# Kernel tuning notes

Measured on AMD Instinct MI355X. Metric: run time of the kernel, lower is better.

The kernel has to match this reference:

```python
import jax, jax.numpy as jnp
import numpy as np

LAM = 0.1       # self.lam
MAX_ITER = 100  # fista_reweighted maxIter
TOL = 1e-5      # convergence tolerance


def creat_dictionary(T, rr, theta):
    # torch creatRealDictionary: row i = [1, rr^i*cos(i*theta), rr^i*sin(i*theta)]
    i = jnp.arange(T, dtype=rr.dtype)[:, None]           # [T,1]
    p = rr[None, :] ** i                                  # [T,P]
    W1 = p * jnp.cos(i * theta[None, :])                  # [T,P]
    W2 = p * jnp.sin(i * theta[None, :])                  # [T,P]
    ones = jnp.ones((T, 1), rr.dtype)
    return jnp.concatenate([ones, W1, W2], axis=1)        # [T, 1+2P]


def fista_reweighted(D, Y, lambd, w):
    # D: [T,K], Y: [N,T,M], w: [N,K,M]
    DtD = D.T @ D                                         # [K,K]
    DtY = jnp.einsum('tk,ntm->nkm', D, Y)                 # [N,K,M]
    # torch.norm(DtD, 2) with no dim = 2-norm of the flattened matrix (Frobenius)
    Linv = 1.0 / jnp.linalg.norm(DtD)
    K = DtD.shape[0]
    A = jnp.eye(K, dtype=D.dtype) - DtD * Linv            # [K,K]
    wl = w * (lambd * Linv)                               # weighted lambda [N,K,M]
    c_minus = DtY * Linv - wl
    c_plus = DtY * Linv + wl
    x0 = jnp.zeros_like(DtY)

    def body(carry, _):
        x_old, y_old, t_old, done = carry
        Ay = jnp.einsum('kj,njm->nkm', A, y_old)
        # shrinkage: max(0, Ay + c-) + min(0, Ay + c+)
        x_new = jnp.maximum(0.0, Ay + c_minus) + jnp.minimum(0.0, Ay + c_plus)
        t_new = (1.0 + jnp.sqrt(1.0 + 4.0 * t_old ** 2)) / 2.0
        tt = (t_old - 1.0) / t_new
        y_new = x_new + tt * (x_new - x_old)
        conv = (jnp.linalg.norm(x_old - x_new) / K) < TOL
        stop = done | conv
        # on convergence torch breaks with x_old = x_new; afterwards freeze state
        x_next = jnp.where(done, x_old, x_new)
        y_next = jnp.where(stop, y_old, y_new)
        t_next = jnp.where(stop, t_old, t_new)
        return (x_next, y_next, t_next, stop), None

    init = (x0, x0, jnp.float32(1.0), jnp.array(False))
    (x, _, _, _), _ = jax.lax.scan(jax.checkpoint(body), init, None, length=MAX_ITER)
    return x


def setup_inputs() -> dict:
    key = jax.random.key(0)
    k1, k2, k3 = jax.random.split(key, 3)
    N, T, M, P = 256, 36, 50, 80
    x = jax.random.normal(k1, (N, T, M), dtype=jnp.float32)
    rr = 0.9 + 0.1 * jax.random.uniform(k2, (P,), dtype=jnp.float32)   # poles near unit circle
    theta = jnp.pi * jax.random.uniform(k3, (P,), dtype=jnp.float32)
    return {"x": x, "rr": rr, "theta": theta, "T": T}


def reference(x, rr, theta, T):
    dic = creat_dictionary(T, rr, theta)                  # [T,K]
    K = dic.shape[1]
    w = jnp.ones((x.shape[0], K, x.shape[2]), x.dtype)    # [N,K,M]
    code = None
    for _ in range(2):                                    # reweighting heuristic, 2 passes
        code = fista_reweighted(dic, x, LAM, w)
        wn = 1.0 / (jnp.abs(code) + 0.01)
        w = wn / jnp.linalg.norm(wn) * K
    reconst = jnp.einsum('tk,nkm->ntm', dic, code)        # [N,T,M]
    return code, dic, reconst
```

## Files before the change

kernel.cpp:

```cpp
#include <hip/hip_runtime.h>
#include <math.h>

#define N_    256
#define T_    36
#define M_    50
#define P_    80
#define K_    161
#define PADK  192
#define KC    12
#define NBR   800
#define NTR   128
#define LAM_  0.1f
#define MAXIT 100

#define KM_     (K_*M_)
#define TM_     (T_*M_)
#define OUT_DIC 2060800
#define OUT_REC 2066596

#define WS_LINV 0
#define WS_D    64
#define WS_ACC  8192
#define WS_WN   9000
#define WS_NIT1 9002
#define WS_NIT2 9003

__global__ __launch_bounds__(256) void k_dict(const float* __restrict__ rr,
                                              const float* __restrict__ th,
                                              float* __restrict__ out,
                                              float* __restrict__ ws) {
    __shared__ float Dl[T_*PADK];
    const int tid = threadIdx.x;
    for (int e = tid; e < T_*PADK; e += 256) {
        int t = e / PADK, k = e - (e / PADK) * PADK;
        float v = 0.f;
        if (k == 0) v = 1.f;
        else if (k <= P_)      { float r = rr[k-1];     float a = th[k-1]*(float)t;
                                 v = powf(r, (float)t) * cosf(a); }
        else if (k <= 2*P_)    { float r = rr[k-1-P_];  float a = th[k-1-P_]*(float)t;
                                 v = powf(r, (float)t) * sinf(a); }
        Dl[e] = v;
        ws[WS_D + e] = v;
        if (k < K_) out[OUT_DIC + t*K_ + k] = v;
    }
    __syncthreads();
    float loc = 0.f;
    for (int e = tid; e < T_*T_; e += 256) {
        int t1 = e / T_, t2 = e - (e / T_) * T_;
        float s = 0.f;
        for (int k = 0; k < K_; ++k) s = fmaf(Dl[t1*PADK+k], Dl[t2*PADK+k], s);
        loc = fmaf(s, s, loc);
    }
    #pragma unroll
    for (int mm = 1; mm < 64; mm <<= 1) loc += __shfl_xor(loc, mm);
    __shared__ float rb[4];
    if ((tid & 63) == 0) rb[tid >> 6] = loc;
    __syncthreads();
    if (tid == 0) {
        float tot = rb[0] + rb[1] + rb[2] + rb[3];
        ws[WS_LINV] = 1.0f / sqrtf(tot);
    }
}

template<int CTRL>
__device__ __forceinline__ float dpp_mov(float v) {
    int p = __builtin_amdgcn_update_dpp(0, __float_as_int(v), CTRL, 0xF, 0xF, true);
    return __int_as_float(p);
}
__device__ __forceinline__ float reduce16(float z) {
    z += dpp_mov<0xB1>(z);
    z += dpp_mov<0x4E>(z);
    z += dpp_mov<0x141>(z);
    z += dpp_mov<0x140>(z);
    return z;
}

template<int PASS>
__global__ __attribute__((amdgpu_flat_work_group_size(NTR, NTR),
                          amdgpu_waves_per_eu(1, 2)))
void k_run(const float* __restrict__ X,
           float* __restrict__ out,
           float* __restrict__ ws) {
    __shared__ __align__(16) float Dl[T_*PADK];
    const int tid = threadIdx.x;
    for (int e = tid; e < T_*PADK; e += NTR) Dl[e] = ws[WS_D + e];
    const float Linv = ws[WS_LINV];
    __syncthreads();

    const int lane  = tid & 63;
    const int sub   = lane & 15;
    const int gw    = (int)blockIdx.x * (NTR/64) + (tid >> 6);
    const int colb  = gw*8 + (lane >> 4)*2;
    const int n0    = colb / M_;
    const int m0    = colb - n0*M_;
    const int n1    = (colb+1) / M_;
    const int m1    = (colb+1) - n1*M_;
    const int kbase = sub * KC;
    const float* Y0 = X + n0*TM_ + m0;
    const float* Y1 = X + n1*TM_ + m1;

    float x[2][KC], y[2][KC], cm[2][KC], cp[2][KC];
    const float wlc = LAM_ * Linv;

    #pragma unroll
    for (int j = 0; j < KC; ++j) { cm[0][j] = 0.f; cm[1][j] = 0.f; }
    #pragma unroll 2
    for (int t = 0; t < T_; ++t) {
        float yv0 = Y0[t*M_], yv1 = Y1[t*M_];
        const float4* dp = (const float4*)(Dl + t*PADK + kbase);
        float4 da[3] = {dp[0], dp[1], dp[2]};
        #pragma unroll
        for (int q = 0; q < 3; ++q) {
            cm[0][4*q+0] = fmaf(da[q].x, yv0, cm[0][4*q+0]);
            cm[0][4*q+1] = fmaf(da[q].y, yv0, cm[0][4*q+1]);
            cm[0][4*q+2] = fmaf(da[q].z, yv0, cm[0][4*q+2]);
            cm[0][4*q+3] = fmaf(da[q].w, yv0, cm[0][4*q+3]);
            cm[1][4*q+0] = fmaf(da[q].x, yv1, cm[1][4*q+0]);
            cm[1][4*q+1] = fmaf(da[q].y, yv1, cm[1][4*q+1]);
            cm[1][4*q+2] = fmaf(da[q].z, yv1, cm[1][4*q+2]);
            cm[1][4*q+3] = fmaf(da[q].w, yv1, cm[1][4*q+3]);
        }
    }
    #pragma unroll
    for (int j = 0; j < KC; ++j) { cm[0][j] *= Linv; cm[1][j] *= Linv; }

    if (PASS == 1) {
        float scale = ((float)K_) * (LAM_ * Linv) / sqrtf(ws[WS_WN]);
        #pragma unroll
        for (int c = 0; c < 2; ++c) {
            const int nn = c ? n1 : n0, mm2 = c ? m1 : m0;
            #pragma unroll
            for (int j = 0; j < KC; ++j) {
                int kg = kbase + j;
                float x1 = (kg < K_) ? out[nn*KM_ + kg*M_ + mm2] : 0.f;
                float wl = scale / (fabsf(x1) + 0.01f);
                float bb = cm[c][j];
                cm[c][j] = bb - wl;
                cp[c][j] = bb + wl;
            }
        }
    }

    float tcur = 1.f;

    auto iterate = [&](float tt) -> float {
        float u[2][KC];
        #pragma unroll
        for (int j = 0; j < KC; ++j) { u[0][j] = 0.f; u[1][j] = 0.f; }
        #pragma unroll 2
        for (int t = 0; t < T_; ++t) {
            const float4* dp = (const float4*)(Dl + t*PADK + kbase);
            float4 da[3] = {dp[0], dp[1], dp[2]};
            float z00=0.f, z01=0.f, z02=0.f, z03=0.f;
            float z10=0.f, z11=0.f, z12=0.f, z13=0.f;
            #pragma unroll
            for (int q = 0; q < 3; ++q) {
                z00 = fmaf(da[q].x, y[0][4*q+0], z00);
                z01 = fmaf(da[q].y, y[0][4*q+1], z01);
                z02 = fmaf(da[q].z, y[0][4*q+2], z02);
                z03 = fmaf(da[q].w, y[0][4*q+3], z03);
                z10 = fmaf(da[q].x, y[1][4*q+0], z10);
                z11 = fmaf(da[q].y, y[1][4*q+1], z11);
                z12 = fmaf(da[q].z, y[1][4*q+2], z12);
                z13 = fmaf(da[q].w, y[1][4*q+3], z13);
            }
            float z0 = reduce16((z00+z01) + (z02+z03));
            float z1 = reduce16((z10+z11) + (z12+z13));
            #pragma unroll
            for (int q = 0; q < 3; ++q) {
                u[0][4*q+0] = fmaf(da[q].x, z0, u[0][4*q+0]);
                u[0][4*q+1] = fmaf(da[q].y, z0, u[0][4*q+1]);
                u[0][4*q+2] = fmaf(da[q].z, z0, u[0][4*q+2]);
                u[0][4*q+3] = fmaf(da[q].w, z0, u[0][4*q+3]);
                u[1][4*q+0] = fmaf(da[q].x, z1, u[1][4*q+0]);
                u[1][4*q+1] = fmaf(da[q].y, z1, u[1][4*q+1]);
                u[1][4*q+2] = fmaf(da[q].z, z1, u[1][4*q+2]);
                u[1][4*q+3] = fmaf(da[q].w, z1, u[1][4*q+3]);
            }
        }
        float ss = 0.f;
        #pragma unroll
        for (int c = 0; c < 2; ++c) {
            #pragma unroll
            for (int j = 0; j < KC; ++j) {
                float v = fmaf(-Linv, u[c][j], y[c][j]);
                float xn;
                if (PASS == 0) {
                    float s = v + cm[c][j];
                    xn = fmaxf(0.f, s - wlc) + fminf(0.f, s + wlc);
                } else {
                    xn = fmaxf(0.f, v + cm[c][j]) + fminf(0.f, v + cp[c][j]);
                }
                float d = xn - x[c][j];
                ss      = fmaf(d, d, ss);
                y[c][j] = fmaf(tt, d, xn);
                x[c][j] = xn;
            }
        }
        return ss;
    };

    #pragma unroll
    for (int j = 0; j < KC; ++j) {
        x[0][j] = 0.f; x[1][j] = 0.f; y[0][j] = 0.f; y[1][j] = 0.f;
    }
    float* acc = ws + WS_ACC + PASS*4*MAXIT;
    for (int i = 0; i < MAXIT; ++i) {
        float tnext = 0.5f * (1.f + sqrtf(fmaf(4.f*tcur, tcur, 1.f)));
        float tt = (tcur - 1.f) / tnext;
        tcur = tnext;
        float ss = iterate(tt);
        ss = reduce16(ss);
        ss += __shfl_xor(ss, 16);
        ss += __shfl_xor(ss, 32);
        if (lane == 0) atomicAdd(acc + i*4 + (gw & 3), ss);
    }

    #pragma unroll
    for (int j = 0; j < KC; ++j) {
        int kg = kbase + j;
        if (kg < K_) {
            out[n0*KM_ + kg*M_ + m0] = x[0][j];
            out[n1*KM_ + kg*M_ + m1] = x[1][j];
        }
    }
}

struct Geo { int n0, m0, n1, m1, kbase, sub, lane; };
__device__ __forceinline__ Geo make_geo() {
    Geo g;
    const int tid = threadIdx.x;
    g.lane = tid & 63;
    g.sub  = g.lane & 15;
    const int gw   = (int)blockIdx.x * (NTR/64) + (tid >> 6);
    const int colb = gw*8 + (g.lane >> 4)*2;
    g.n0 = colb / M_;       g.m0 = colb - g.n0*M_;
    g.n1 = (colb+1) / M_;   g.m1 = (colb+1) - g.n1*M_;
    g.kbase = g.sub * KC;
    return g;
}

__device__ __forceinline__ void compute_b(const float* Dl, int kbase, float Linv,
                                          const float* Y0, const float* Y1,
                                          float (&b)[2][KC]) {
    #pragma unroll
    for (int j = 0; j < KC; ++j) { b[0][j] = 0.f; b[1][j] = 0.f; }
    #pragma unroll 2
    for (int t = 0; t < T_; ++t) {
        float yv0 = Y0[t*M_], yv1 = Y1[t*M_];
        const float4* dp = (const float4*)(Dl + t*PADK + kbase);
        float4 da[3] = {dp[0], dp[1], dp[2]};
        #pragma unroll
        for (int q = 0; q < 3; ++q) {
            b[0][4*q+0] = fmaf(da[q].x, yv0, b[0][4*q+0]);
            b[0][4*q+1] = fmaf(da[q].y, yv0, b[0][4*q+1]);
            b[0][4*q+2] = fmaf(da[q].z, yv0, b[0][4*q+2]);
            b[0][4*q+3] = fmaf(da[q].w, yv0, b[0][4*q+3]);
            b[1][4*q+0] = fmaf(da[q].x, yv1, b[1][4*q+0]);
            b[1][4*q+1] = fmaf(da[q].y, yv1, b[1][4*q+1]);
            b[1][4*q+2] = fmaf(da[q].z, yv1, b[1][4*q+2]);
            b[1][4*q+3] = fmaf(da[q].w, yv1, b[1][4*q+3]);
        }
    }
    #pragma unroll
    for (int j = 0; j < KC; ++j) { b[0][j] *= Linv; b[1][j] *= Linv; }
}

__device__ __forceinline__ void run_fista(const float* Dl, int kbase, float Linv,
                                          const float (&cmv)[2][KC],
                                          const float (&cpv)[2][KC],
                                          float (&x)[2][KC], int nit) {
    float y[2][KC];
    #pragma unroll
    for (int j = 0; j < KC; ++j) {
        x[0][j] = 0.f; x[1][j] = 0.f; y[0][j] = 0.f; y[1][j] = 0.f;
    }
    float tcur = 1.f;
    for (int i = 0; i < nit; ++i) {
        float tnext = 0.5f * (1.f + sqrtf(fmaf(4.f*tcur, tcur, 1.f)));
        float tt = (tcur - 1.f) / tnext;
        tcur = tnext;
        float u[2][KC];
        #pragma unroll
        for (int j = 0; j < KC; ++j) { u[0][j] = 0.f; u[1][j] = 0.f; }
        #pragma unroll 2
        for (int t = 0; t < T_; ++t) {
            const float4* dp = (const float4*)(Dl + t*PADK + kbase);
            float4 da[3] = {dp[0], dp[1], dp[2]};
            float z00=0.f, z01=0.f, z02=0.f, z03=0.f;
            float z10=0.f, z11=0.f, z12=0.f, z13=0.f;
            #pragma unroll
            for (int q = 0; q < 3; ++q) {
                z00 = fmaf(da[q].x, y[0][4*q+0], z00);
                z01 = fmaf(da[q].y, y[0][4*q+1], z01);
                z02 = fmaf(da[q].z, y[0][4*q+2], z02);
                z03 = fmaf(da[q].w, y[0][4*q+3], z03);
                z10 = fmaf(da[q].x, y[1][4*q+0], z10);
                z11 = fmaf(da[q].y, y[1][4*q+1], z11);
                z12 = fmaf(da[q].z, y[1][4*q+2], z12);
                z13 = fmaf(da[q].w, y[1][4*q+3], z13);
            }
            float z0 = reduce16((z00+z01) + (z02+z03));
            float z1 = reduce16((z10+z11) + (z12+z13));
            #pragma unroll
            for (int q = 0; q < 3; ++q) {
                u[0][4*q+0] = fmaf(da[q].x, z0, u[0][4*q+0]);
                u[0][4*q+1] = fmaf(da[q].y, z0, u[0][4*q+1]);
                u[0][4*q+2] = fmaf(da[q].z, z0, u[0][4*q+2]);
                u[0][4*q+3] = fmaf(da[q].w, z0, u[0][4*q+3]);
                u[1][4*q+0] = fmaf(da[q].x, z1, u[1][4*q+0]);
                u[1][4*q+1] = fmaf(da[q].y, z1, u[1][4*q+1]);
                u[1][4*q+2] = fmaf(da[q].z, z1, u[1][4*q+2]);
                u[1][4*q+3] = fmaf(da[q].w, z1, u[1][4*q+3]);
            }
        }
        #pragma unroll
        for (int c = 0; c < 2; ++c) {
            #pragma unroll
            for (int j = 0; j < KC; ++j) {
                float v = fmaf(-Linv, u[c][j], y[c][j]);
                float xn = fmaxf(0.f, v + cmv[c][j]) + fminf(0.f, v + cpv[c][j]);
                float d = xn - x[c][j];
                y[c][j] = fmaf(tt, d, xn);
                x[c][j] = xn;
            }
        }
    }
}

__device__ __forceinline__ void write_code_g(const Geo& g, const float (&x)[2][KC],
                                             float* out) {
    #pragma unroll
    for (int j = 0; j < KC; ++j) {
        int kg = g.kbase + j;
        if (kg < K_) {
            out[g.n0*KM_ + kg*M_ + g.m0] = x[0][j];
            out[g.n1*KM_ + kg*M_ + g.m1] = x[1][j];
        }
    }
}
__device__ __forceinline__ void load_code_g(const Geo& g, float (&x)[2][KC],
                                            const float* out) {
    #pragma unroll
    for (int j = 0; j < KC; ++j) {
        int kg = g.kbase + j;
        x[0][j] = (kg < K_) ? out[g.n0*KM_ + kg*M_ + g.m0] : 0.f;
        x[1][j] = (kg < K_) ? out[g.n1*KM_ + kg*M_ + g.m1] : 0.f;
    }
}

__global__ void k_scan(float* __restrict__ ws, int pass) {
    const float THR2 = (1e-5f * (float)K_) * (1e-5f * (float)K_);
    int lane = threadIdx.x;
    const float* acc = ws + WS_ACC + pass*4*MAXIT;
    int best = MAXIT + 1;
    for (int i = lane; i < MAXIT; i += 64) {
        float a = (acc[i*4] + acc[i*4+1]) + (acc[i*4+2] + acc[i*4+3]);
        if (a < THR2) best = min(best, i + 1);
    }
    #pragma unroll
    for (int mm = 1; mm < 64; mm <<= 1) best = min(best, __shfl_xor(best, mm));
    if (lane == 0) ((int*)ws)[pass == 0 ? WS_NIT1 : WS_NIT2] = best;
}

__global__ __launch_bounds__(NTR, 1) void k_fin1(const float* __restrict__ X,
                                                 float* __restrict__ out,
                                                 float* __restrict__ ws) {
    __shared__ __align__(16) float Dl[T_*PADK];
    for (int e = threadIdx.x; e < T_*PADK; e += NTR) Dl[e] = ws[WS_D + e];
    const float Linv = ws[WS_LINV];
    __syncthreads();

    Geo g = make_geo();
    const int nit1 = ((const int*)ws)[WS_NIT1];
    float x[2][KC];

    if (nit1 <= MAXIT) {
        float b[2][KC], cmv[2][KC], cpv[2][KC];
        compute_b(Dl, g.kbase, Linv, X + g.n0*TM_ + g.m0, X + g.n1*TM_ + g.m1, b);
        const float wlc = LAM_ * Linv;
        #pragma unroll
        for (int c = 0; c < 2; ++c)
            #pragma unroll
            for (int j = 0; j < KC; ++j) { cmv[c][j] = b[c][j] - wlc;
                                           cpv[c][j] = b[c][j] + wlc; }
        run_fista(Dl, g.kbase, Linv, cmv, cpv, x, nit1);
        write_code_g(g, x, out);
    } else {
        load_code_g(g, x, out);
    }

    float loc = 0.f;
    #pragma unroll
    for (int c = 0; c < 2; ++c)
        #pragma unroll
        for (int j = 0; j < KC; ++j) {
            if (g.kbase + j < K_) {
                float wn = 1.0f / (fabsf(x[c][j]) + 0.01f);
                loc = fmaf(wn, wn, loc);
            }
        }
    #pragma unroll
    for (int mm = 1; mm < 64; mm <<= 1) loc += __shfl_xor(loc, mm);
    if (g.lane == 0) atomicAdd(ws + WS_WN, loc);
}

__global__ __launch_bounds__(NTR, 1) void k_fin2(const float* __restrict__ X,
                                                 float* __restrict__ out,
                                                 float* __restrict__ ws) {
    __shared__ __align__(16) float Dl[T_*PADK];
    for (int e = threadIdx.x; e < T_*PADK; e += NTR) Dl[e] = ws[WS_D + e];
    const float Linv = ws[WS_LINV];
    __syncthreads();

    Geo g = make_geo();
    const int nit1 = ((const int*)ws)[WS_NIT1];
    const int nit2 = ((const int*)ws)[WS_NIT2];
    float x[2][KC];

    if (nit2 <= MAXIT) {
        float b[2][KC], cmv[2][KC], cpv[2][KC];
        compute_b(Dl, g.kbase, Linv, X + g.n0*TM_ + g.m0, X + g.n1*TM_ + g.m1, b);
        const float wlc = LAM_ * Linv;
        #pragma unroll
        for (int c = 0; c < 2; ++c)
            #pragma unroll
            for (int j = 0; j < KC; ++j) { cmv[c][j] = b[c][j] - wlc;
                                           cpv[c][j] = b[c][j] + wlc; }
        int nrep1 = nit1 <= MAXIT ? nit1 : MAXIT;
        run_fista(Dl, g.kbase, Linv, cmv, cpv, x, nrep1);
        float scale = ((float)K_) * (LAM_ * Linv) / sqrtf(ws[WS_WN]);
        #pragma unroll
        for (int c = 0; c < 2; ++c)
            #pragma unroll
            for (int j = 0; j < KC; ++j) {
                float wl = scale / (fabsf(x[c][j]) + 0.01f);
                cmv[c][j] = b[c][j] - wl;
                cpv[c][j] = b[c][j] + wl;
            }
        run_fista(Dl, g.kbase, Linv, cmv, cpv, x, nit2);
        write_code_g(g, x, out);
    } else {
        load_code_g(g, x, out);
    }

    #pragma unroll 2
    for (int t = 0; t < T_; ++t) {
        const float4* dp = (const float4*)(Dl + t*PADK + g.kbase);
        float4 da[3] = {dp[0], dp[1], dp[2]};
        float z00=0.f, z01=0.f, z02=0.f, z03=0.f;
        float z10=0.f, z11=0.f, z12=0.f, z13=0.f;
        #pragma unroll
        for (int q = 0; q < 3; ++q) {
            z00 = fmaf(da[q].x, x[0][4*q+0], z00);
            z01 = fmaf(da[q].y, x[0][4*q+1], z01);
            z02 = fmaf(da[q].z, x[0][4*q+2], z02);
            z03 = fmaf(da[q].w, x[0][4*q+3], z03);
            z10 = fmaf(da[q].x, x[1][4*q+0], z10);
            z11 = fmaf(da[q].y, x[1][4*q+1], z11);
            z12 = fmaf(da[q].z, x[1][4*q+2], z12);
            z13 = fmaf(da[q].w, x[1][4*q+3], z13);
        }
        float z0 = reduce16((z00+z01) + (z02+z03));
        float z1 = reduce16((z10+z11) + (z12+z13));
        if (g.sub == (t & 15)) {
            out[OUT_REC + g.n0*TM_ + t*M_ + g.m0] = z0;
            out[OUT_REC + g.n1*TM_ + t*M_ + g.m1] = z1;
        }
    }
}

extern "C" void kernel_launch(void* const* d_in, const int* in_sizes, int n_in,
                              void* d_out, int out_size, void* d_ws, size_t ws_size,
                              hipStream_t stream) {
    const float* X  = (const float*)d_in[0];
    const float* rr = (const float*)d_in[1];
    const float* th = (const float*)d_in[2];
    float* out = (float*)d_out;
    float* ws  = (float*)d_ws;

    hipMemsetAsync((char*)d_ws + WS_ACC*sizeof(float), 0, 4096, stream);
    k_dict  <<<dim3(1),   dim3(256), 0, stream>>>(rr, th, out, ws);
    k_run<0><<<dim3(NBR), dim3(NTR), 0, stream>>>(X, out, ws);
    k_scan  <<<dim3(1),   dim3(64),  0, stream>>>(ws, 0);
    k_fin1  <<<dim3(NBR), dim3(NTR), 0, stream>>>(X, out, ws);
    k_run<1><<<dim3(NBR), dim3(NTR), 0, stream>>>(X, out, ws);
    k_scan  <<<dim3(1),   dim3(64),  0, stream>>>(ws, 1);
    k_fin2  <<<dim3(NBR), dim3(NTR), 0, stream>>>(X, out, ws);
}
```

Measured before the change: 1.793 ms.

## Split each column's K dimension across 32 lanes with 6 atoms per lane

Each column pair's 161 dictionary atoms are now spread over 32 lanes holding 6 coefficients each, instead of 16 lanes holding 12. Block size doubles to 256 threads, and the dictionary is stored in a padded per-lane layout (stride 8, 256 per row) so each lane reads a float4 plus a float2. The goal is to cut per-thread register use and serial FMA work per iteration so occupancy rises, and waves_per_eu is raised to match. The cost is one extra cross-lane shuffle step in every reduction and half as many columns per wave.

New measurement: 2.432 ms. 1.36x slower.

```diff
diff --git a/kernel.cpp b/kernel.cpp
--- a/kernel.cpp
+++ b/kernel.cpp
@@ -6,10 +6,11 @@
 #define M_    50
 #define P_    80
 #define K_    161
-#define PADK  192
-#define KC    12
+#define LKC   6
+#define LSTR  8
+#define DROW  256
 #define NBR   800
-#define NTR   128
+#define NTR   256
 #define LAM_  0.1f
 #define MAXIT 100
 
@@ -20,35 +21,40 @@
 
 #define WS_LINV 0
 #define WS_D    64
-#define WS_ACC  8192
-#define WS_WN   9000
-#define WS_NIT1 9002
-#define WS_NIT2 9003
+#define WS_ACC  9472
+#define WS_WN   10272
+#define WS_NIT1 10274
+#define WS_NIT2 10275
 
 __global__ __launch_bounds__(256) void k_dict(const float* __restrict__ rr,
                                               const float* __restrict__ th,
                                               float* __restrict__ out,
                                               float* __restrict__ ws) {
-    __shared__ float Dl[T_*PADK];
+    __shared__ float Dl[T_*K_];
     const int tid = threadIdx.x;
-    for (int e = tid; e < T_*PADK; e += 256) {
-        int t = e / PADK, k = e - (e / PADK) * PADK;
-        float v = 0.f;
+    for (int e = tid; e < T_*K_; e += 256) {
+        int t = e / K_, k = e - (e / K_) * K_;
+        float v;
         if (k == 0) v = 1.f;
         else if (k <= P_)      { float r = rr[k-1];     float a = th[k-1]*(float)t;
                                  v = powf(r, (float)t) * cosf(a); }
-        else if (k <= 2*P_)    { float r = rr[k-1-P_];  float a = th[k-1-P_]*(float)t;
+        else                   { float r = rr[k-1-P_];  float a = th[k-1-P_]*(float)t;
                                  v = powf(r, (float)t) * sinf(a); }
         Dl[e] = v;
-        ws[WS_D + e] = v;
-        if (k < K_) out[OUT_DIC + t*K_ + k] = v;
+        out[OUT_DIC + t*K_ + k] = v;
     }
     __syncthreads();
+    for (int e = tid; e < T_*DROW; e += 256) {
+        int t = e >> 8, s = e & 255;
+        int sub = s >> 3, j = s & 7;
+        int kg = sub*LKC + j;
+        ws[WS_D + e] = (j < LKC && kg < K_) ? Dl[t*K_ + kg] : 0.f;
+    }
     float loc = 0.f;
     for (int e = tid; e < T_*T_; e += 256) {
         int t1 = e / T_, t2 = e - (e / T_) * T_;
         float s = 0.f;
-        for (int k = 0; k < K_; ++k) s = fmaf(Dl[t1*PADK+k], Dl[t2*PADK+k], s);
+        for (int k = 0; k < K_; ++k) s = fmaf(Dl[t1*K_+k], Dl[t2*K_+k], s);
         loc = fmaf(s, s, loc);
     }
     #pragma unroll
@@ -67,71 +73,78 @@
     int p = __builtin_amdgcn_update_dpp(0, __float_as_int(v), CTRL, 0xF, 0xF, true);
     return __int_as_float(p);
 }
-__device__ __forceinline__ float reduce16(float z) {
+__device__ __forceinline__ float reduce16v(float z) {
     z += dpp_mov<0xB1>(z);
     z += dpp_mov<0x4E>(z);
     z += dpp_mov<0x141>(z);
     z += dpp_mov<0x140>(z);
     return z;
 }
+__device__ __forceinline__ float reduce32v(float z) {
+    z = reduce16v(z);
+    z += __shfl_xor(z, 16);
+    return z;
+}
+
+struct Geo { int n0, m0, n1, m1, sub, lane, gw, lofs; };
+__device__ __forceinline__ Geo make_geo() {
+    Geo g;
+    const int tid = threadIdx.x;
+    g.lane = tid & 63;
+    g.sub  = g.lane & 31;
+    g.gw   = (int)blockIdx.x * (NTR/64) + (tid >> 6);
+    const int colb = g.gw*4 + (g.lane >> 5)*2;
+    g.n0 = colb / M_;       g.m0 = colb - g.n0*M_;
+    g.n1 = (colb+1) / M_;   g.m1 = (colb+1) - g.n1*M_;
+    g.lofs = g.sub * LSTR;
+    return g;
+}
 
 template<int PASS>
 __global__ __attribute__((amdgpu_flat_work_group_size(NTR, NTR),
-                          amdgpu_waves_per_eu(1, 2)))
+                          amdgpu_waves_per_eu(2, 3)))
 void k_run(const float* __restrict__ X,
            float* __restrict__ out,
            float* __restrict__ ws) {
-    __shared__ __align__(16) float Dl[T_*PADK];
+    __shared__ __align__(16) float Dl[T_*DROW];
     const int tid = threadIdx.x;
-    for (int e = tid; e < T_*PADK; e += NTR) Dl[e] = ws[WS_D + e];
+    for (int e = tid; e < T_*DROW; e += NTR) Dl[e] = ws[WS_D + e];
     const float Linv = ws[WS_LINV];
     __syncthreads();
 
-    const int lane  = tid & 63;
-    const int sub   = lane & 15;
-    const int gw    = (int)blockIdx.x * (NTR/64) + (tid >> 6);
-    const int colb  = gw*8 + (lane >> 4)*2;
-    const int n0    = colb / M_;
-    const int m0    = colb - n0*M_;
-    const int n1    = (colb+1) / M_;
-    const int m1    = (colb+1) - n1*M_;
-    const int kbase = sub * KC;
-    const float* Y0 = X + n0*TM_ + m0;
-    const float* Y1 = X + n1*TM_ + m1;
-
-    float x[2][KC], y[2][KC], cm[2][KC], cp[2][KC];
+    Geo g = make_geo();
+    const float* Y0 = X + g.n0*TM_ + g.m0;
+    const float* Y1 = X + g.n1*TM_ + g.m1;
+
+    float x[2][LKC], y[2][LKC], cm[2][LKC], cp[2][LKC];
     const float wlc = LAM_ * Linv;
 
     #pragma unroll
-    for (int j = 0; j < KC; ++j) { cm[0][j] = 0.f; cm[1][j] = 0.f; }
+    for (int j = 0; j < LKC; ++j) { cm[0][j] = 0.f; cm[1][j] = 0.f; }
     #pragma unroll 2
     for (int t = 0; t < T_; ++t) {
         float yv0 = Y0[t*M_], yv1 = Y1[t*M_];
-        const float4* dp = (const float4*)(Dl + t*PADK + kbase);
-        float4 da[3] = {dp[0], dp[1], dp[2]};
-        #pragma unroll
-        for (int q = 0; q < 3; ++q) {
-            cm[0][4*q+0] = fmaf(da[q].x, yv0, cm[0][4*q+0]);
-            cm[0][4*q+1] = fmaf(da[q].y, yv0, cm[0][4*q+1]);
-            cm[0][4*q+2] = fmaf(da[q].z, yv0, cm[0][4*q+2]);
-            cm[0][4*q+3] = fmaf(da[q].w, yv0, cm[0][4*q+3]);
-            cm[1][4*q+0] = fmaf(da[q].x, yv1, cm[1][4*q+0]);
-            cm[1][4*q+1] = fmaf(da[q].y, yv1, cm[1][4*q+1]);
-            cm[1][4*q+2] = fmaf(da[q].z, yv1, cm[1][4*q+2]);
-            cm[1][4*q+3] = fmaf(da[q].w, yv1, cm[1][4*q+3]);
-        }
-    }
-    #pragma unroll
-    for (int j = 0; j < KC; ++j) { cm[0][j] *= Linv; cm[1][j] *= Linv; }
+        const float* dr = Dl + t*DROW + g.lofs;
+        float4 d01 = *(const float4*)dr;
+        float2 d2  = *(const float2*)(dr + 4);
+        float da[LKC] = {d01.x, d01.y, d01.z, d01.w, d2.x, d2.y};
+        #pragma unroll
+        for (int j = 0; j < LKC; ++j) {
+            cm[0][j] = fmaf(da[j], yv0, cm[0][j]);
+            cm[1][j] = fmaf(da[j], yv1, cm[1][j]);
+        }
+    }
+    #pragma unroll
+    for (int j = 0; j < LKC; ++j) { cm[0][j] *= Linv; cm[1][j] *= Linv; }
 
     if (PASS == 1) {
         float scale = ((float)K_) * (LAM_ * Linv) / sqrtf(ws[WS_WN]);
         #pragma unroll
         for (int c = 0; c < 2; ++c) {
-            const int nn = c ? n1 : n0, mm2 = c ? m1 : m0;
-            #pragma unroll
-            for (int j = 0; j < KC; ++j) {
-                int kg = kbase + j;
+            const int nn = c ? g.n1 : g.n0, mm2 = c ? g.m1 : g.m0;
+            #pragma unroll
+            for (int j = 0; j < LKC; ++j) {
+                int kg = g.sub*LKC + j;
                 float x1 = (kg < K_) ? out[nn*KM_ + kg*M_ + mm2] : 0.f;
                 float wl = scale / (fabsf(x1) + 0.01f);
                 float bb = cm[c][j];
@@ -144,45 +157,34 @@
     float tcur = 1.f;
 
     auto iterate = [&](float tt) -> float {
-        float u[2][KC];
-        #pragma unroll
-        for (int j = 0; j < KC; ++j) { u[0][j] = 0.f; u[1][j] = 0.f; }
+        float u[2][LKC];
+        #pragma unroll
+        for (int j = 0; j < LKC; ++j) { u[0][j] = 0.f; u[1][j] = 0.f; }
         #pragma unroll 2
         for (int t = 0; t < T_; ++t) {
-            const float4* dp = (const float4*)(Dl + t*PADK + kbase);
-            float4 da[3] = {dp[0], dp[1], dp[2]};
-            float z00=0.f, z01=0.f, z02=0.f, z03=0.f;
-            float z10=0.f, z11=0.f, z12=0.f, z13=0.f;
-            #pragma unroll
-            for (int q = 0; q < 3; ++q) {
-                z00 = fmaf(da[q].x, y[0][4*q+0], z00);
-                z01 = fmaf(da[q].y, y[0][4*q+1], z01);
-                z02 = fmaf(da[q].z, y[0][4*q+2], z02);
-                z03 = fmaf(da[q].w, y[0][4*q+3], z03);
-                z10 = fmaf(da[q].x, y[1][4*q+0], z10);
-                z11 = fmaf(da[q].y, y[1][4*q+1], z11);
-                z12 = fmaf(da[q].z, y[1][4*q+2], z12);
-                z13 = fmaf(da[q].w, y[1][4*q+3], z13);
-            }
-            float z0 = reduce16((z00+z01) + (z02+z03));
-            float z1 = reduce16((z10+z11) + (z12+z13));
-            #pragma unroll
-            for (int q = 0; q < 3; ++q) {
-                u[0][4*q+0] = fmaf(da[q].x, z0, u[0][4*q+0]);
-                u[0][4*q+1] = fmaf(da[q].y, z0, u[0][4*q+1]);
-                u[0][4*q+2] = fmaf(da[q].z, z0, u[0][4*q+2]);
-                u[0][4*q+3] = fmaf(da[q].w, z0, u[0][4*q+3]);
-                u[1][4*q+0] = fmaf(da[q].x, z1, u[1][4*q+0]);
-                u[1][4*q+1] = fmaf(da[q].y, z1, u[1][4*q+1]);
-                u[1][4*q+2] = fmaf(da[q].z, z1, u[1][4*q+2]);
-                u[1][4*q+3] = fmaf(da[q].w, z1, u[1][4*q+3]);
+            const float* dr = Dl + t*DROW + g.lofs;
+            float4 d01 = *(const float4*)dr;
+            float2 d2  = *(const float2*)(dr + 4);
+            float da[LKC] = {d01.x, d01.y, d01.z, d01.w, d2.x, d2.y};
+            float z0 = 0.f, z1 = 0.f;
+            #pragma unroll
+            for (int j = 0; j < LKC; ++j) {
+                z0 = fmaf(da[j], y[0][j], z0);
+                z1 = fmaf(da[j], y[1][j], z1);
+            }
+            z0 = reduce32v(z0);
+            z1 = reduce32v(z1);
+            #pragma unroll
+            for (int j = 0; j < LKC; ++j) {
+                u[0][j] = fmaf(da[j], z0, u[0][j]);
+                u[1][j] = fmaf(da[j], z1, u[1][j]);
             }
         }
         float ss = 0.f;
         #pragma unroll
         for (int c = 0; c < 2; ++c) {
             #pragma unroll
-            for (int j = 0; j < KC; ++j) {
+            for (int j = 0; j < LKC; ++j) {
                 float v = fmaf(-Linv, u[c][j], y[c][j]);
                 float xn;
                 if (PASS == 0) {
@@ -201,7 +203,7 @@
     };
 
     #pragma unroll
-    for (int j = 0; j < KC; ++j) {
+    for (int j = 0; j < LKC; ++j) {
         x[0][j] = 0.f; x[1][j] = 0.f; y[0][j] = 0.f; y[1][j] = 0.f;
     }
     float* acc = ws + WS_ACC + PASS*4*MAXIT;
@@ -210,69 +212,51 @@
         float tt = (tcur - 1.f) / tnext;
         tcur = tnext;
         float ss = iterate(tt);
-        ss = reduce16(ss);
+        ss = reduce16v(ss);
         ss += __shfl_xor(ss, 16);
         ss += __shfl_xor(ss, 32);
-        if (lane == 0) atomicAdd(acc + i*4 + (gw & 3), ss);
-    }
-
-    #pragma unroll
-    for (int j = 0; j < KC; ++j) {
-        int kg = kbase + j;
+        if (g.lane == 0) atomicAdd(acc + i*4 + (g.gw & 3), ss);
+    }
+
+    #pragma unroll
+    for (int j = 0; j < LKC; ++j) {
+        int kg = g.sub*LKC + j;
         if (kg < K_) {
-            out[n0*KM_ + kg*M_ + m0] = x[0][j];
-            out[n1*KM_ + kg*M_ + m1] = x[1][j];
-        }
-    }
-}
-
-struct Geo { int n0, m0, n1, m1, kbase, sub, lane; };
-__device__ __forceinline__ Geo make_geo() {
-    Geo g;
-    const int tid = threadIdx.x;
-    g.lane = tid & 63;
-    g.sub  = g.lane & 15;
-    const int gw   = (int)blockIdx.x * (NTR/64) + (tid >> 6);
-    const int colb = gw*8 + (g.lane >> 4)*2;
-    g.n0 = colb / M_;       g.m0 = colb - g.n0*M_;
-    g.n1 = (colb+1) / M_;   g.m1 = (colb+1) - g.n1*M_;
-    g.kbase = g.sub * KC;
-    return g;
-}
-
-__device__ __forceinline__ void compute_b(const float* Dl, int kbase, float Linv,
+            out[g.n0*KM_ + kg*M_ + g.m0] = x[0][j];
+            out[g.n1*KM_ + kg*M_ + g.m1] = x[1][j];
+        }
+    }
+}
+
+__device__ __forceinline__ void compute_b(const float* Dl, int lofs, float Linv,
                                           const float* Y0, const float* Y1,
-                                          float (&b)[2][KC]) {
-    #pragma unroll
-    for (int j = 0; j < KC; ++j) { b[0][j] = 0.f; b[1][j] = 0.f; }
+                                          float (&b)[2][LKC]) {
+    #pragma unroll
+    for (int j = 0; j < LKC; ++j) { b[0][j] = 0.f; b[1][j] = 0.f; }
     #pragma unroll 2
     for (int t = 0; t < T_; ++t) {
         float yv0 = Y0[t*M_], yv1 = Y1[t*M_];
-        const float4* dp = (const float4*)(Dl + t*PADK + kbase);
-        float4 da[3] = {dp[0], dp[1], dp[2]};
-        #pragma unroll
-        for (int q = 0; q < 3; ++q) {
-            b[0][4*q+0] = fmaf(da[q].x, yv0, b[0][4*q+0]);
-            b[0][4*q+1] = fmaf(da[q].y, yv0, b[0][4*q+1]);
-            b[0][4*q+2] = fmaf(da[q].z, yv0, b[0][4*q+2]);
-            b[0][4*q+3] = fmaf(da[q].w, yv0, b[0][4*q+3]);
-            b[1][4*q+0] = fmaf(da[q].x, yv1, b[1][4*q+0]);
-            b[1][4*q+1] = fmaf(da[q].y, yv1, b[1][4*q+1]);
-            b[1][4*q+2] = fmaf(da[q].z, yv1, b[1][4*q+2]);
-            b[1][4*q+3] = fmaf(da[q].w, yv1, b[1][4*q+3]);
-        }
-    }
-    #pragma unroll
-    for (int j = 0; j < KC; ++j) { b[0][j] *= Linv; b[1][j] *= Linv; }
-}
-
-__device__ __forceinline__ void run_fista(const float* Dl, int kbase, float Linv,
-                                          const float (&cmv)[2][KC],
-                                          const float (&cpv)[2][KC],
-                                          float (&x)[2][KC], int nit) {
-    float y[2][KC];
-    #pragma unroll
-    for (int j = 0; j < KC; ++j) {
+        const float* dr = Dl + t*DROW + lofs;
+        float4 d01 = *(const float4*)dr;
+        float2 d2  = *(const float2*)(dr + 4);
+        float da[LKC] = {d01.x, d01.y, d01.z, d01.w, d2.x, d2.y};
+        #pragma unroll
+        for (int j = 0; j < LKC; ++j) {
+            b[0][j] = fmaf(da[j], yv0, b[0][j]);
+            b[1][j] = fmaf(da[j], yv1, b[1][j]);
+        }
+    }
+    #pragma unroll
+    for (int j = 0; j < LKC; ++j) { b[0][j] *= Linv; b[1][j] *= Linv; }
+}
+
+__device__ __forceinline__ void run_fista(const float* Dl, int lofs, float Linv,
+                                          const float (&cmv)[2][LKC],
+                                          const float (&cpv)[2][LKC],
+                                          float (&x)[2][LKC], int nit) {
+    float y[2][LKC];
+    #pragma unroll
+    for (int j = 0; j < LKC; ++j) {
         x[0][j] = 0.f; x[1][j] = 0.f; y[0][j] = 0.f; y[1][j] = 0.f;
     }
     float tcur = 1.f;
@@ -280,44 +264,33 @@
         float tnext = 0.5f * (1.f + sqrtf(fmaf(4.f*tcur, tcur, 1.f)));
         float tt = (tcur - 1.f) / tnext;
         tcur = tnext;
-        float u[2][KC];
-        #pragma unroll
-        for (int j = 0; j < KC; ++j) { u[0][j] = 0.f; u[1][j] = 0.f; }
+        float u[2][LKC];
+        #pragma unroll
+        for (int j = 0; j < LKC; ++j) { u[0][j] = 0.f; u[1][j] = 0.f; }
         #pragma unroll 2
         for (int t = 0; t < T_; ++t) {
-            const float4* dp = (const float4*)(Dl + t*PADK + kbase);
-            float4 da[3] = {dp[0], dp[1], dp[2]};
-            float z00=0.f, z01=0.f, z02=0.f, z03=0.f;
-            float z10=0.f, z11=0.f, z12=0.f, z13=0.f;
-            #pragma unroll
-            for (int q = 0; q < 3; ++q) {
-                z00 = fmaf(da[q].x, y[0][4*q+0], z00);
-                z01 = fmaf(da[q].y, y[0][4*q+1], z01);
-                z02 = fmaf(da[q].z, y[0][4*q+2], z02);
-                z03 = fmaf(da[q].w, y[0][4*q+3], z03);
-                z10 = fmaf(da[q].x, y[1][4*q+0], z10);
-                z11 = fmaf(da[q].y, y[1][4*q+1], z11);
-                z12 = fmaf(da[q].z, y[1][4*q+2], z12);
-                z13 = fmaf(da[q].w, y[1][4*q+3], z13);
-            }
-            float z0 = reduce16((z00+z01) + (z02+z03));
-            float z1 = reduce16((z10+z11) + (z12+z13));
-            #pragma unroll
-            for (int q = 0; q < 3; ++q) {
-                u[0][4*q+0] = fmaf(da[q].x, z0, u[0][4*q+0]);
-                u[0][4*q+1] = fmaf(da[q].y, z0, u[0][4*q+1]);
-                u[0][4*q+2] = fmaf(da[q].z, z0, u[0][4*q+2]);
-                u[0][4*q+3] = fmaf(da[q].w, z0, u[0][4*q+3]);
-                u[1][4*q+0] = fmaf(da[q].x, z1, u[1][4*q+0]);
-                u[1][4*q+1] = fmaf(da[q].y, z1, u[1][4*q+1]);
-                u[1][4*q+2] = fmaf(da[q].z, z1, u[1][4*q+2]);
-                u[1][4*q+3] = fmaf(da[q].w, z1, u[1][4*q+3]);
+            const float* dr = Dl + t*DROW + lofs;
+            float4 d01 = *(const float4*)dr;
+            float2 d2  = *(const float2*)(dr + 4);
+            float da[LKC] = {d01.x, d01.y, d01.z, d01.w, d2.x, d2.y};
+            float z0 = 0.f, z1 = 0.f;
+            #pragma unroll
+            for (int j = 0; j < LKC; ++j) {
+                z0 = fmaf(da[j], y[0][j], z0);
+                z1 = fmaf(da[j], y[1][j], z1);
+            }
+            z0 = reduce32v(z0);
+            z1 = reduce32v(z1);
+            #pragma unroll
+            for (int j = 0; j < LKC; ++j) {
+                u[0][j] = fmaf(da[j], z0, u[0][j]);
+                u[1][j] = fmaf(da[j], z1, u[1][j]);
             }
         }
         #pragma unroll
         for (int c = 0; c < 2; ++c) {
             #pragma unroll
-            for (int j = 0; j < KC; ++j) {
+            for (int j = 0; j < LKC; ++j) {
                 float v = fmaf(-Linv, u[c][j], y[c][j]);
                 float xn = fmaxf(0.f, v + cmv[c][j]) + fminf(0.f, v + cpv[c][j]);
                 float d = xn - x[c][j];
@@ -328,22 +301,22 @@
     }
 }
 
-__device__ __forceinline__ void write_code_g(const Geo& g, const float (&x)[2][KC],
+__device__ __forceinline__ void write_code_g(const Geo& g, const float (&x)[2][LKC],
                                              float* out) {
     #pragma unroll
-    for (int j = 0; j < KC; ++j) {
-        int kg = g.kbase + j;
+    for (int j = 0; j < LKC; ++j) {
+        int kg = g.sub*LKC + j;
         if (kg < K_) {
             out[g.n0*KM_ + kg*M_ + g.m0] = x[0][j];
             out[g.n1*KM_ + kg*M_ + g.m1] = x[1][j];
         }
     }
 }
-__device__ __forceinline__ void load_code_g(const Geo& g, float (&x)[2][KC],
+__device__ __forceinline__ void load_code_g(const Geo& g, float (&x)[2][LKC],
                                             const float* out) {
     #pragma unroll
-    for (int j = 0; j < KC; ++j) {
-        int kg = g.kbase + j;
+    for (int j = 0; j < LKC; ++j) {
+        int kg = g.sub*LKC + j;
         x[0][j] = (kg < K_) ? out[g.n0*KM_ + kg*M_ + g.m0] : 0.f;
         x[1][j] = (kg < K_) ? out[g.n1*KM_ + kg*M_ + g.m1] : 0.f;
     }
@@ -366,25 +339,25 @@
 __global__ __launch_bounds__(NTR, 1) void k_fin1(const float* __restrict__ X,
                                                  float* __restrict__ out,
                                                  float* __restrict__ ws) {
-    __shared__ __align__(16) float Dl[T_*PADK];
-    for (int e = threadIdx.x; e < T_*PADK; e += NTR) Dl[e] = ws[WS_D + e];
+    __shared__ __align__(16) float Dl[T_*DROW];
+    for (int e = threadIdx.x; e < T_*DROW; e += NTR) Dl[e] = ws[WS_D + e];
     const float Linv = ws[WS_LINV];
     __syncthreads();
 
     Geo g = make_geo();
     const int nit1 = ((const int*)ws)[WS_NIT1];
-    float x[2][KC];
+    float x[2][LKC];
 
     if (nit1 <= MAXIT) {
-        float b[2][KC], cmv[2][KC], cpv[2][KC];
-        compute_b(Dl, g.kbase, Linv, X + g.n0*TM_ + g.m0, X + g.n1*TM_ + g.m1, b);
+        float b[2][LKC], cmv[2][LKC], cpv[2][LKC];
+        compute_b(Dl, g.lofs, Linv, X + g.n0*TM_ + g.m0, X + g.n1*TM_ + g.m1, b);
         const float wlc = LAM_ * Linv;
         #pragma unroll
         for (int c = 0; c < 2; ++c)
             #pragma unroll
-            for (int j = 0; j < KC; ++j) { cmv[c][j] = b[c][j] - wlc;
-                                           cpv[c][j] = b[c][j] + wlc; }
-        run_fista(Dl, g.kbase, Linv, cmv, cpv, x, nit1);
+            for (int j = 0; j < LKC; ++j) { cmv[c][j] = b[c][j] - wlc;
+                                            cpv[c][j] = b[c][j] + wlc; }
+        run_fista(Dl, g.lofs, Linv, cmv, cpv, x, nit1);
         write_code_g(g, x, out);
     } else {
         load_code_g(g, x, out);
@@ -394,8 +367,8 @@
     #pragma unroll
     for (int c = 0; c < 2; ++c)
         #pragma unroll
-        for (int j = 0; j < KC; ++j) {
-            if (g.kbase + j < K_) {
+        for (int j = 0; j < LKC; ++j) {
+            if (g.sub*LKC + j < K_) {
                 float wn = 1.0f / (fabsf(x[c][j]) + 0.01f);
                 loc = fmaf(wn, wn, loc);
             }
@@ -408,37 +381,37 @@
 __global__ __launch_bounds__(NTR, 1) void k_fin2(const float* __restrict__ X,
                                                  float* __restrict__ out,
                                                  float* __restrict__ ws) {
-    __shared__ __align__(16) float Dl[T_*PADK];
-    for (int e = threadIdx.x; e < T_*PADK; e += NTR) Dl[e] = ws[WS_D + e];
+    __shared__ __align__(16) float Dl[T_*DROW];
+    for (int e = threadIdx.x; e < T_*DROW; e += NTR) Dl[e] = ws[WS_D + e];
     const float Linv = ws[WS_LINV];
     __syncthreads();
 
     Geo g = make_geo();
     const int nit1 = ((const int*)ws)[WS_NIT1];
     const int nit2 = ((const int*)ws)[WS_NIT2];
-    float x[2][KC];
+    float x[2][LKC];
 
     if (nit2 <= MAXIT) {
-        float b[2][KC], cmv[2][KC], cpv[2][KC];
-        compute_b(Dl, g.kbase, Linv, X + g.n0*TM_ + g.m0, X + g.n1*TM_ + g.m1, b);
+        float b[2][LKC], cmv[2][LKC], cpv[2][LKC];
+        compute_b(Dl, g.lofs, Linv, X + g.n0*TM_ + g.m0, X + g.n1*TM_ + g.m1, b);
         const float wlc = LAM_ * Linv;
         #pragma unroll
         for (int c = 0; c < 2; ++c)
             #pragma unroll
-            for (int j = 0; j < KC; ++j) { cmv[c][j] = b[c][j] - wlc;
-                                           cpv[c][j] = b[c][j] + wlc; }
+            for (int j = 0; j < LKC; ++j) { cmv[c][j] = b[c][j] - wlc;
+                                            cpv[c][j] = b[c][j] + wlc; }
         int nrep1 = nit1 <= MAXIT ? nit1 : MAXIT;
-        run_fista(Dl, g.kbase, Linv, cmv, cpv, x, nrep1);
+        run_fista(Dl, g.lofs, Linv, cmv, cpv, x, nrep1);
         float scale = ((float)K_) * (LAM_ * Linv) / sqrtf(ws[WS_WN]);
         #pragma unroll
         for (int c = 0; c < 2; ++c)
             #pragma unroll
-            for (int j = 0; j < KC; ++j) {
+            for (int j = 0; j < LKC; ++j) {
                 float wl = scale / (fabsf(x[c][j]) + 0.01f);
                 cmv[c][j] = b[c][j] - wl;
                 cpv[c][j] = b[c][j] + wl;
             }
-        run_fista(Dl, g.kbase, Linv, cmv, cpv, x, nit2);
+        run_fista(Dl, g.lofs, Linv, cmv, cpv, x, nit2);
         write_code_g(g, x, out);
     } else {
         load_code_g(g, x, out);
@@ -446,24 +419,19 @@
 
     #pragma unroll 2
     for (int t = 0; t < T_; ++t) {
-        const float4* dp = (const float4*)(Dl + t*PADK + g.kbase);
-        float4 da[3] = {dp[0], dp[1], dp[2]};
-        float z00=0.f, z01=0.f, z02=0.f, z03=0.f;
-        float z10=0.f, z11=0.f, z12=0.f, z13=0.f;
-        #pragma unroll
-        for (int q = 0; q < 3; ++q) {
-            z00 = fmaf(da[q].x, x[0][4*q+0], z00);
-            z01 = fmaf(da[q].y, x[0][4*q+1], z01);
-            z02 = fmaf(da[q].z, x[0][4*q+2], z02);
-            z03 = fmaf(da[q].w, x[0][4*q+3], z03);
-            z10 = fmaf(da[q].x, x[1][4*q+0], z10);
-            z11 = fmaf(da[q].y, x[1][4*q+1], z11);
-            z12 = fmaf(da[q].z, x[1][4*q+2], z12);
-            z13 = fmaf(da[q].w, x[1][4*q+3], z13);
-        }
-        float z0 = reduce16((z00+z01) + (z02+z03));
-        float z1 = reduce16((z10+z11) + (z12+z13));
-        if (g.sub == (t & 15)) {
+        const float* dr = Dl + t*DROW + g.lofs;
+        float4 d01 = *(const float4*)dr;
+        float2 d2  = *(const float2*)(dr + 4);
+        float da[LKC] = {d01.x, d01.y, d01.z, d01.w, d2.x, d2.y};
+        float z0 = 0.f, z1 = 0.f;
+        #pragma unroll
+        for (int j = 0; j < LKC; ++j) {
+            z0 = fmaf(da[j], x[0][j], z0);
+            z1 = fmaf(da[j], x[1][j], z1);
+        }
+        z0 = reduce32v(z0);
+        z1 = reduce32v(z1);
+        if (g.sub == (t & 31)) {
             out[OUT_REC + g.n0*TM_ + t*M_ + g.m0] = z0;
             out[OUT_REC + g.n1*TM_ + t*M_ + g.m1] = z1;
         }
```
